# Kernel optimization log

Hardware: AMD Instinct MI355X
Metric: run time of the kernel (lower is better)

## Reference

```python
import jax, jax.numpy as jnp
import numpy as np

EPS = 1e-6
SIGMA = 0.02  # inverse-quadratic kernel scale (RGBuvHistBlock default)
H_BINS = 128


def _rgb_uv_hist(x, mu):
    # x: [B, 3, H, W] in [0, 1]; mu: [h] bin centers in [-3, 3]
    x = jnp.clip(x, 0.0, 1.0)
    B = x.shape[0]
    I = x.reshape(B, 3, -1)                       # [B, 3, N]
    Iy = jnp.sqrt(jnp.sum(I * I, axis=1) + EPS)   # [B, N] intensity scaling
    logI = jnp.log(I + EPS)                       # [B, 3, N]

    def kern(d):
        # inverse-quadratic kernel: 1 / (1 + (|d| / sigma)^2)
        return 1.0 / (1.0 + (d / SIGMA) ** 2)

    def chan(c0, c1, c2):
        Iu = logI[:, c0] - logI[:, c1]            # [B, N]
        Iv = logI[:, c0] - logI[:, c2]            # [B, N]
        du = kern(jnp.abs(Iu[:, :, None] - mu[None, None, :]))  # [B, N, h]
        dv = kern(jnp.abs(Iv[:, :, None] - mu[None, None, :]))  # [B, N, h]
        a = Iy[:, :, None] * du                   # [B, N, h]
        return jnp.einsum('bnu,bnv->buv', a, dv)  # [B, h, h]

    # channel order: r vs (g,b), g vs (r,b), b vs (r,g)
    hists = jnp.stack([chan(0, 1, 2), chan(1, 0, 2), chan(2, 0, 1)], axis=1)  # [B,3,h,h]
    norm = jnp.sum(hists, axis=(1, 2, 3)).reshape(-1, 1, 1, 1) + EPS
    return hists / norm


def setup_inputs() -> dict:
    key = jax.random.key(0)
    k1, k2 = jax.random.split(key)
    B, C, H, W = 4, 3, 256, 256
    pred = jax.random.uniform(k1, (B, C, H, W), dtype=jnp.float32)
    target = jax.random.uniform(k2, (B, C, H, W), dtype=jnp.float32)
    return {"pred": pred, "target": target}


def reference(pred, target):
    mu = jnp.linspace(-3.0, 3.0, H_BINS, dtype=pred.dtype)
    pred_hist = _rgb_uv_hist(pred, mu)
    target_hist = _rgb_uv_hist(target, mu)
    diff = jnp.sqrt(target_hist) - jnp.sqrt(pred_hist)
    return (1.0 / np.sqrt(2.0)) * jnp.sqrt(jnp.sum(diff * diff)) / pred_hist.shape[0]
```

## Files before the change

### kernel.cpp

```cpp
#include <hip/hip_runtime.h>

#define NPIX   65536
#define HB     128
#define EPSF   1e-6f
#define NCOMB  24
#define ROWB   80
#define MATB   (HB * ROWB)
#define BUFB   (3 * MATB)
#define PPW    24576

typedef _Float16 half8  __attribute__((ext_vector_type(8)));
typedef __fp16   fp16x2 __attribute__((ext_vector_type(2)));
typedef float    f32x16 __attribute__((ext_vector_type(16)));
typedef float    f32x2  __attribute__((ext_vector_type(2)));

__device__ __forceinline__ unsigned pk2(float a, float b) {
    union { fp16x2 h; unsigned u; } cv;
    cv.h = __builtin_amdgcn_cvt_pkrtz(a, b);
    return cv.u;
}

__global__ __launch_bounds__(256, 2) void hist_mfma(
    const float* __restrict__ pred, const float* __restrict__ tgt,
    unsigned* __restrict__ parts, int nchunk)
{
    __shared__ char smat[2 * BUFB];

    const int t    = threadIdx.x;
    const int lane = t & 63;
    const int wave = t >> 6;
    const int chunk = blockIdx.x % nchunk;
    const int ib    = blockIdx.x / nchunk;
    const int b     = ib & 3;
    const int img   = ib >> 2;
    const int kchunk = NPIX / nchunk;
    const int nreg   = kchunk >> 5;

    const float* __restrict__ base = (img ? tgt : pred) + (size_t)b * 3 * NPIX;
    const float* __restrict__ Rp = base;
    const float* __restrict__ Gp = base + NPIX;
    const float* __restrict__ Bp = base + 2 * NPIX;

    const int   i16     = lane & 15;
    const int   r4      = lane >> 4;
    const int   rowbase = wave * 4 + r4;
    const float MU0     = (float)rowbase * (300.0f / 127.0f) - 150.0f;
    const float MUSTEP  = 16.0f * (300.0f / 127.0f);
    char* genp0 = smat + rowbase * ROWB + i16 * 4;
    char* genp1 = genp0 + BUFB;

    const int ti2 = wave >> 1;
    const int tj2 = wave & 1;

    f32x16 acc[3][2][2];
#pragma unroll
    for (int g = 0; g < 3; ++g)
#pragma unroll
        for (int i = 0; i < 2; ++i)
#pragma unroll
            for (int j = 0; j < 2; ++j)
#pragma unroll
                for (int r = 0; r < 16; ++r) acc[g][i][j][r] = 0.0f;

    const int n0 = chunk * kchunk;

    f32x2 Ra, Ga, Ba, Rb, Gb, Bb;
    f32x2 ddrg, ddrb, ddgb, rw2;

    auto issue_ld = [&](int reg, f32x2& R, f32x2& G, f32x2& B) {
        const int n = n0 + reg * 32 + 2 * i16;
        R = *reinterpret_cast<const f32x2*>(Rp + n);
        G = *reinterpret_cast<const f32x2*>(Gp + n);
        B = *reinterpret_cast<const f32x2*>(Bp + n);
    };

    auto scalars = [&](f32x2 R, f32x2 G, f32x2 B) {
        const float C = 34.65735902799726547086f;
        float r0 = fminf(fmaxf(R.x, 0.0f), 1.0f);
        float r1 = fminf(fmaxf(R.y, 0.0f), 1.0f);
        float g0 = fminf(fmaxf(G.x, 0.0f), 1.0f);
        float g1 = fminf(fmaxf(G.y, 0.0f), 1.0f);
        float b0 = fminf(fmaxf(B.x, 0.0f), 1.0f);
        float b1 = fminf(fmaxf(B.y, 0.0f), 1.0f);
        float lr0 = __builtin_amdgcn_logf(r0 + EPSF);
        float lr1 = __builtin_amdgcn_logf(r1 + EPSF);
        float lg0 = __builtin_amdgcn_logf(g0 + EPSF);
        float lg1 = __builtin_amdgcn_logf(g1 + EPSF);
        float lb0 = __builtin_amdgcn_logf(b0 + EPSF);
        float lb1 = __builtin_amdgcn_logf(b1 + EPSF);
        ddrg.x = (lr0 - lg0) * C;  ddrg.y = (lr1 - lg1) * C;
        ddrb.x = (lr0 - lb0) * C;  ddrb.y = (lr1 - lb1) * C;
        ddgb.x = (lg0 - lb0) * C;  ddgb.y = (lg1 - lb1) * C;
        const float s0 = __builtin_fmaf(r0, r0,
                          __builtin_fmaf(g0, g0,
                           __builtin_fmaf(b0, b0, EPSF)));
        const float s1 = __builtin_fmaf(r1, r1,
                          __builtin_fmaf(g1, g1,
                           __builtin_fmaf(b1, b1, EPSF)));
        rw2.x = __builtin_amdgcn_sqrtf(__builtin_amdgcn_sqrtf(s0));
        rw2.y = __builtin_amdgcn_sqrtf(__builtin_amdgcn_sqrtf(s1));
    };

    auto gen_mat = [&](char* bp, int mat, f32x2 dd) {
        float m = MU0;
#pragma unroll
        for (int s = 0; s < 8; ++s) {
            const float ex = dd.x - m, ey = dd.y - m;
            const float tx = __builtin_fmaf(ex, ex, 1.0f);
            const float ty = __builtin_fmaf(ey, ey, 1.0f);
            const float vx = __builtin_amdgcn_rcpf(tx) * rw2.x;
            const float vy = __builtin_amdgcn_rcpf(ty) * rw2.y;
            *reinterpret_cast<unsigned*>(bp + mat * MATB + s * 16 * ROWB)
                = pk2(vx, vy);
            m += MUSTEP;
        }
    };

    auto rd = [&](const char* mp, int matid, int row, int koff) -> half8 {
        return *reinterpret_cast<const half8*>(mp + matid * MATB
                                               + row * ROWB + koff);
    };

    auto body = [&](const char* mp, char* gp, bool dogen) {
        const int kbase = (lane >> 5) << 4;
        const int r0 = ti2 * 64 + (lane & 31);
        const int c0 = tj2 * 64 + (lane & 31);

        if (dogen) gen_mat(gp, 0, ddrg);
        {
            half8 a0 = rd(mp, 0, r0,      kbase);
            half8 a1 = rd(mp, 0, r0 + 32, kbase);
            half8 p0 = rd(mp, 1, c0,      kbase);
            half8 p1 = rd(mp, 1, c0 + 32, kbase);
            __builtin_amdgcn_s_setprio(1);
            acc[0][0][0] = __builtin_amdgcn_mfma_f32_32x32x16_f16(a0, p0, acc[0][0][0], 0, 0, 0);
            acc[0][0][1] = __builtin_amdgcn_mfma_f32_32x32x16_f16(a0, p1, acc[0][0][1], 0, 0, 0);
            acc[0][1][0] = __builtin_amdgcn_mfma_f32_32x32x16_f16(a1, p0, acc[0][1][0], 0, 0, 0);
            acc[0][1][1] = __builtin_amdgcn_mfma_f32_32x32x16_f16(a1, p1, acc[0][1][1], 0, 0, 0);
            __builtin_amdgcn_s_setprio(0);

            if (dogen) gen_mat(gp, 1, ddrb);
            half8 q0  = rd(mp, 2, c0,      kbase);
            half8 q1  = rd(mp, 2, c0 + 32, kbase);
            half8 bb0 = rd(mp, 1, r0,      kbase);
            half8 bb1 = rd(mp, 1, r0 + 32, kbase);
            __builtin_amdgcn_s_setprio(1);
            acc[1][0][0] = __builtin_amdgcn_mfma_f32_32x32x16_f16(a0, q0, acc[1][0][0], 0, 0, 0);
            acc[1][0][1] = __builtin_amdgcn_mfma_f32_32x32x16_f16(a0, q1, acc[1][0][1], 0, 0, 0);
            acc[1][1][0] = __builtin_amdgcn_mfma_f32_32x32x16_f16(a1, q0, acc[1][1][0], 0, 0, 0);
            acc[1][1][1] = __builtin_amdgcn_mfma_f32_32x32x16_f16(a1, q1, acc[1][1][1], 0, 0, 0);
            acc[2][0][0] = __builtin_amdgcn_mfma_f32_32x32x16_f16(bb0, q0, acc[2][0][0], 0, 0, 0);
            acc[2][0][1] = __builtin_amdgcn_mfma_f32_32x32x16_f16(bb0, q1, acc[2][0][1], 0, 0, 0);
            acc[2][1][0] = __builtin_amdgcn_mfma_f32_32x32x16_f16(bb1, q0, acc[2][1][0], 0, 0, 0);
            acc[2][1][1] = __builtin_amdgcn_mfma_f32_32x32x16_f16(bb1, q1, acc[2][1][1], 0, 0, 0);
            __builtin_amdgcn_s_setprio(0);
        }

        if (dogen) gen_mat(gp, 2, ddgb);
        {
            const int k1 = 32 + kbase;
            half8 a0  = rd(mp, 0, r0,      k1);
            half8 a1  = rd(mp, 0, r0 + 32, k1);
            half8 p0  = rd(mp, 1, c0,      k1);
            half8 p1  = rd(mp, 1, c0 + 32, k1);
            half8 q0  = rd(mp, 2, c0,      k1);
            half8 q1  = rd(mp, 2, c0 + 32, k1);
            half8 bb0 = rd(mp, 1, r0,      k1);
            half8 bb1 = rd(mp, 1, r0 + 32, k1);
            __builtin_amdgcn_s_setprio(1);
            acc[0][0][0] = __builtin_amdgcn_mfma_f32_32x32x16_f16(a0, p0, acc[0][0][0], 0, 0, 0);
            acc[0][0][1] = __builtin_amdgcn_mfma_f32_32x32x16_f16(a0, p1, acc[0][0][1], 0, 0, 0);
            acc[0][1][0] = __builtin_amdgcn_mfma_f32_32x32x16_f16(a1, p0, acc[0][1][0], 0, 0, 0);
            acc[0][1][1] = __builtin_amdgcn_mfma_f32_32x32x16_f16(a1, p1, acc[0][1][1], 0, 0, 0);
            acc[1][0][0] = __builtin_amdgcn_mfma_f32_32x32x16_f16(a0, q0, acc[1][0][0], 0, 0, 0);
            acc[1][0][1] = __builtin_amdgcn_mfma_f32_32x32x16_f16(a0, q1, acc[1][0][1], 0, 0, 0);
            acc[1][1][0] = __builtin_amdgcn_mfma_f32_32x32x16_f16(a1, q0, acc[1][1][0], 0, 0, 0);
            acc[1][1][1] = __builtin_amdgcn_mfma_f32_32x32x16_f16(a1, q1, acc[1][1][1], 0, 0, 0);
            acc[2][0][0] = __builtin_amdgcn_mfma_f32_32x32x16_f16(bb0, q0, acc[2][0][0], 0, 0, 0);
            acc[2][0][1] = __builtin_amdgcn_mfma_f32_32x32x16_f16(bb0, q1, acc[2][0][1], 0, 0, 0);
            acc[2][1][0] = __builtin_amdgcn_mfma_f32_32x32x16_f16(bb1, q0, acc[2][1][0], 0, 0, 0);
            acc[2][1][1] = __builtin_amdgcn_mfma_f32_32x32x16_f16(bb1, q1, acc[2][1][1], 0, 0, 0);
            __builtin_amdgcn_s_setprio(0);
        }
    };

    issue_ld(0, Ra, Ga, Ba);
    scalars(Ra, Ga, Ba);
    gen_mat(genp0, 0, ddrg);
    gen_mat(genp0, 1, ddrb);
    gen_mat(genp0, 2, ddgb);
    issue_ld(1, Rb, Gb, Bb);
    __syncthreads();

    for (int rg = 0; rg < nreg; rg += 2) {
        scalars(Rb, Gb, Bb);
        issue_ld(min(rg + 2, nreg - 1), Ra, Ga, Ba);
        body(smat, genp1, true);
        __syncthreads();
        scalars(Ra, Ga, Ba);
        issue_ld(min(rg + 3, nreg - 1), Rb, Gb, Bb);
        body(smat + BUFB, genp0, rg + 2 < nreg);
        __syncthreads();
    }

    unsigned* pb0 = parts + (size_t)blockIdx.x * PPW;
#pragma unroll
    for (int g = 0; g < 3; ++g)
#pragma unroll
        for (int i2 = 0; i2 < 2; ++i2)
#pragma unroll
            for (int j2 = 0; j2 < 2; ++j2) {
                unsigned* wp = pb0
                    + (size_t)((((g * 4 + wave) * 2 + i2) * 2 + j2) * 8) * 64
                    + lane;
#pragma unroll
                for (int rh = 0; rh < 8; ++rh)
                    wp[rh * 64] = pk2(acc[g][i2][j2][2 * rh],
                                      acc[g][i2][j2][2 * rh + 1]);
            }
}

__global__ __launch_bounds__(256) void reduce_norms(
    const unsigned* __restrict__ parts, float* __restrict__ hist,
    float* __restrict__ norms, int nchunk)
{
    const int i    = blockIdx.x * 256 + threadIdx.x;
    const int comb = i >> 13;
    const int rest = i & 8191;
    const int ib   = comb / 3;
    const int g    = comb % 3;
    const unsigned* p = parts + (size_t)(ib * nchunk) * PPW + g * 8192 + rest;
    float s0 = 0.0f, s1 = 0.0f;
    for (int k = 0; k < nchunk; ++k) {
        union { unsigned u; fp16x2 h; } cv;
        cv.u = p[(size_t)k * PPW];
        s0 += (float)cv.h.x;
        s1 += (float)cv.h.y;
    }
    f32x2 o; o.x = s0; o.y = s1;
    *reinterpret_cast<f32x2*>(hist + 2 * (size_t)i) = o;
    float s = s0 + s1;
    for (int o2 = 32; o2 > 0; o2 >>= 1) s += __shfl_down(s, o2, 64);
    __shared__ float wsum[4];
    if ((threadIdx.x & 63) == 0) wsum[threadIdx.x >> 6] = s;
    __syncthreads();
    if (threadIdx.x == 0)
        atomicAdd(&norms[ib], wsum[0] + wsum[1] + wsum[2] + wsum[3]);
}

__global__ __launch_bounds__(256) void loss_k(
    const float* __restrict__ hist, const float* __restrict__ norms,
    float* __restrict__ acc)
{
    const int i  = blockIdx.x * 256 + threadIdx.x;
    const int bb = i / (3 * HB * HB);
    const float rp = __builtin_amdgcn_rcpf(norms[bb] + EPSF);
    const float rt = __builtin_amdgcn_rcpf(norms[4 + bb] + EPSF);
    const float p  = hist[i];
    const float tt = hist[12 * HB * HB + i];
    const float d  = __builtin_amdgcn_sqrtf(tt * rt)
                   - __builtin_amdgcn_sqrtf(p * rp);
    float s = d * d;
    for (int o = 32; o > 0; o >>= 1) s += __shfl_down(s, o, 64);
    __shared__ float wsum[4];
    if ((threadIdx.x & 63) == 0) wsum[threadIdx.x >> 6] = s;
    __syncthreads();
    if (threadIdx.x == 0) atomicAdd(acc, wsum[0] + wsum[1] + wsum[2] + wsum[3]);
}

__global__ void final_k(const float* __restrict__ acc, float* __restrict__ out)
{
    out[0] = __builtin_amdgcn_sqrtf(acc[0]) * 0.70710678118654752440f * 0.25f;
}

extern "C" void kernel_launch(void* const* d_in, const int* in_sizes, int n_in,
                              void* d_out, int out_size, void* d_ws, size_t ws_size,
                              hipStream_t stream)
{
    const float* pred = (const float*)d_in[0];
    const float* tgt  = (const float*)d_in[1];
    float* ws  = (float*)d_ws;
    float* out = (float*)d_out;

    float*    hist  = ws;
    float*    norms = ws + 393216;
    float*    acc   = ws + 393224;
    unsigned* parts = (unsigned*)(ws + 393232);

    int nchunk = 64;
    while (nchunk > 1) {
        const size_t need =
            (393232 + (size_t)8 * nchunk * PPW) * sizeof(float);
        if (need <= ws_size) break;
        nchunk >>= 1;
    }

    (void)hipMemsetAsync(norms, 0, 9 * sizeof(float), stream);

    hist_mfma<<<8 * nchunk, 256, 0, stream>>>(pred, tgt, parts, nchunk);
    reduce_norms<<<NCOMB * HB * HB / 2 / 256, 256, 0, stream>>>(parts, hist,
                                                                norms, nchunk);
    loss_k<<<(4 * 3 * HB * HB) / 256, 256, 0, stream>>>(hist, norms, acc);
    final_k<<<1, 1, 0, stream>>>(acc, out);
}
```

Before: 120.9 us.

## Fold norm sums into histogram kernel and fuse reduction with loss

The histogram kernel now sums its fp32 accumulators per block and atomically adds them into the per-image norms, so the separate norm pass is no longer needed. The partial-reduction and loss kernels are merged: each thread sums pred and target partials across chunks, then computes the sqrt difference directly, with no float histogram buffer written and read back. This drops one kernel launch and the intermediate histogram traffic. One behavioural change: the norms now come from unrounded fp32 accumulators rather than from the fp16-rounded partials, which shifts numerics slightly.

```diff
diff --git a/kernel.cpp b/kernel.cpp
--- a/kernel.cpp
+++ b/kernel.cpp
@@ -3,7 +3,6 @@
 #define NPIX   65536
 #define HB     128
 #define EPSF   1e-6f
-#define NCOMB  24
 #define ROWB   80
 #define MATB   (HB * ROWB)
 #define BUFB   (3 * MATB)
@@ -22,7 +21,7 @@
 
 __global__ __launch_bounds__(256, 2) void hist_mfma(
     const float* __restrict__ pred, const float* __restrict__ tgt,
-    unsigned* __restrict__ parts, int nchunk)
+    unsigned* __restrict__ parts, float* __restrict__ norms, int nchunk)
 {
     __shared__ char smat[2 * BUFB];
 
@@ -204,6 +203,7 @@
     }
 
     unsigned* pb0 = parts + (size_t)blockIdx.x * PPW;
+    float blksum = 0.0f;
 #pragma unroll
     for (int g = 0; g < 3; ++g)
 #pragma unroll
@@ -214,53 +214,61 @@
                     + (size_t)((((g * 4 + wave) * 2 + i2) * 2 + j2) * 8) * 64
                     + lane;
 #pragma unroll
-                for (int rh = 0; rh < 8; ++rh)
+                for (int rh = 0; rh < 8; ++rh) {
                     wp[rh * 64] = pk2(acc[g][i2][j2][2 * rh],
                                       acc[g][i2][j2][2 * rh + 1]);
+                    blksum += acc[g][i2][j2][2 * rh]
+                            + acc[g][i2][j2][2 * rh + 1];
+                }
             }
-}
-
-__global__ __launch_bounds__(256) void reduce_norms(
-    const unsigned* __restrict__ parts, float* __restrict__ hist,
-    float* __restrict__ norms, int nchunk)
+
+    for (int o = 32; o > 0; o >>= 1) blksum += __shfl_down(blksum, o, 64);
+    __shared__ float wsum[4];
+    if (lane == 0) wsum[wave] = blksum;
+    __syncthreads();
+    if (t == 0)
+        atomicAdd(&norms[ib], wsum[0] + wsum[1] + wsum[2] + wsum[3]);
+}
+
+__global__ __launch_bounds__(256) void reduce_loss(
+    const unsigned* __restrict__ parts, const float* __restrict__ norms,
+    float* __restrict__ acc, int nchunk)
 {
-    const int i    = blockIdx.x * 256 + threadIdx.x;
-    const int comb = i >> 13;
-    const int rest = i & 8191;
-    const int ib   = comb / 3;
-    const int g    = comb % 3;
-    const unsigned* p = parts + (size_t)(ib * nchunk) * PPW + g * 8192 + rest;
-    float s0 = 0.0f, s1 = 0.0f;
-    for (int k = 0; k < nchunk; ++k) {
-        union { unsigned u; fp16x2 h; } cv;
-        cv.u = p[(size_t)k * PPW];
-        s0 += (float)cv.h.x;
-        s1 += (float)cv.h.y;
+    const int i      = blockIdx.x * 256 + threadIdx.x;
+    const int comb12 = i >> 13;
+    const int rest   = i & 8191;
+    const int b      = comb12 / 3;
+    const int g      = comb12 % 3;
+    const unsigned* pp = parts + (size_t)(b * nchunk) * PPW + g * 8192 + rest;
+    const unsigned* pt = parts + (size_t)((4 + b) * nchunk) * PPW + g * 8192 + rest;
+
+    float hp0 = 0.0f, hp1 = 0.0f, ht0 = 0.0f, ht1 = 0.0f;
+    int k = 0;
+    for (; k + 8 <= nchunk; k += 8) {
+#pragma unroll
+        for (int j = 0; j < 8; ++j) {
+            union { unsigned u; fp16x2 h; } a, c;
+            a.u = pp[(size_t)(k + j) * PPW];
+            c.u = pt[(size_t)(k + j) * PPW];
+            hp0 += (float)a.h.x;  hp1 += (float)a.h.y;
+            ht0 += (float)c.h.x;  ht1 += (float)c.h.y;
+        }
     }
-    f32x2 o; o.x = s0; o.y = s1;
-    *reinterpret_cast<f32x2*>(hist + 2 * (size_t)i) = o;
-    float s = s0 + s1;
-    for (int o2 = 32; o2 > 0; o2 >>= 1) s += __shfl_down(s, o2, 64);
-    __shared__ float wsum[4];
-    if ((threadIdx.x & 63) == 0) wsum[threadIdx.x >> 6] = s;
-    __syncthreads();
-    if (threadIdx.x == 0)
-        atomicAdd(&norms[ib], wsum[0] + wsum[1] + wsum[2] + wsum[3]);
-}
-
-__global__ __launch_bounds__(256) void loss_k(
-    const float* __restrict__ hist, const float* __restrict__ norms,
-    float* __restrict__ acc)
-{
-    const int i  = blockIdx.x * 256 + threadIdx.x;
-    const int bb = i / (3 * HB * HB);
-    const float rp = __builtin_amdgcn_rcpf(norms[bb] + EPSF);
-    const float rt = __builtin_amdgcn_rcpf(norms[4 + bb] + EPSF);
-    const float p  = hist[i];
-    const float tt = hist[12 * HB * HB + i];
-    const float d  = __builtin_amdgcn_sqrtf(tt * rt)
-                   - __builtin_amdgcn_sqrtf(p * rp);
-    float s = d * d;
+    for (; k < nchunk; ++k) {
+        union { unsigned u; fp16x2 h; } a, c;
+        a.u = pp[(size_t)k * PPW];
+        c.u = pt[(size_t)k * PPW];
+        hp0 += (float)a.h.x;  hp1 += (float)a.h.y;
+        ht0 += (float)c.h.x;  ht1 += (float)c.h.y;
+    }
+
+    const float rp = __builtin_amdgcn_rcpf(norms[b] + EPSF);
+    const float rt = __builtin_amdgcn_rcpf(norms[4 + b] + EPSF);
+    const float d0 = __builtin_amdgcn_sqrtf(ht0 * rt)
+                   - __builtin_amdgcn_sqrtf(hp0 * rp);
+    const float d1 = __builtin_amdgcn_sqrtf(ht1 * rt)
+                   - __builtin_amdgcn_sqrtf(hp1 * rp);
+    float s = __builtin_fmaf(d0, d0, d1 * d1);
     for (int o = 32; o > 0; o >>= 1) s += __shfl_down(s, o, 64);
     __shared__ float wsum[4];
     if ((threadIdx.x & 63) == 0) wsum[threadIdx.x >> 6] = s;
@@ -282,24 +290,20 @@
     float* ws  = (float*)d_ws;
     float* out = (float*)d_out;
 
-    float*    hist  = ws;
-    float*    norms = ws + 393216;
-    float*    acc   = ws + 393224;
-    unsigned* parts = (unsigned*)(ws + 393232);
+    float*    norms = ws;
+    float*    acc   = ws + 8;
+    unsigned* parts = (unsigned*)(ws + 16);
 
     int nchunk = 64;
     while (nchunk > 1) {
-        const size_t need =
-            (393232 + (size_t)8 * nchunk * PPW) * sizeof(float);
+        const size_t need = (16 + (size_t)8 * nchunk * PPW) * sizeof(float);
         if (need <= ws_size) break;
         nchunk >>= 1;
     }
 
-    (void)hipMemsetAsync(norms, 0, 9 * sizeof(float), stream);
-
-    hist_mfma<<<8 * nchunk, 256, 0, stream>>>(pred, tgt, parts, nchunk);
-    reduce_norms<<<NCOMB * HB * HB / 2 / 256, 256, 0, stream>>>(parts, hist,
-                                                                norms, nchunk);
-    loss_k<<<(4 * 3 * HB * HB) / 256, 256, 0, stream>>>(hist, norms, acc);
+    (void)hipMemsetAsync(ws, 0, 9 * sizeof(float), stream);
+
+    hist_mfma<<<8 * nchunk, 256, 0, stream>>>(pred, tgt, parts, norms, nchunk);
+    reduce_loss<<<12 * 8192 / 256, 256, 0, stream>>>(parts, norms, acc, nchunk);
     final_k<<<1, 1, 0, stream>>>(acc, out);
 }
```

After: 99.46 us. 1.22x faster.
